# Kernel tuning notes

Measured on AMD Instinct MI355X. Metric: run time of the kernel, lower is better.

## Reference

```python
import jax, jax.numpy as jnp
import numpy as np

N, D, E, R = 50000, 128, 640000, 500
BN_EPS = 1e-3  # keras BatchNormalization default
L2_EPS = 1e-12  # tf.nn.l2_normalize default


def setup_inputs() -> dict:
    key = jax.random.key(0)
    ks = jax.random.split(key, 10)
    rows = jnp.sort(jax.random.randint(ks[0], (E,), 0, N, dtype=jnp.int32))
    cols = jax.random.randint(ks[1], (E,), 0, N, dtype=jnp.int32)
    return {
        "x": jax.random.normal(ks[2], (N, D), dtype=jnp.float32),
        "rows": rows,
        "cols": cols,
        "adj_vals": jax.random.uniform(ks[3], (E,), dtype=jnp.float32),
        "rel_ids": jax.random.randint(ks[4], (E,), 0, R, dtype=jnp.int32),
        "gamma1": jnp.ones((D,), jnp.float32),
        "beta1": jnp.zeros((D,), jnp.float32),
        "mean1": jnp.zeros((D,), jnp.float32),
        "var1": jnp.ones((D,), jnp.float32),
        "W1": jax.random.normal(ks[5], (D, D), dtype=jnp.float32) * 0.05,
        "b1": jnp.zeros((D,), jnp.float32),
        "gamma2": jnp.ones((D,), jnp.float32),
        "beta2": jnp.zeros((D,), jnp.float32),
        "mean2": jnp.zeros((D,), jnp.float32),
        "var2": jnp.ones((D,), jnp.float32),
        "relation_coeffs": jax.random.uniform(ks[6], (R,), dtype=jnp.float32),
        "coeff_kernel": jax.random.normal(ks[7], (N, 1), dtype=jnp.float32) * 0.05,
        "Wd": jax.random.normal(ks[8], (D, D), dtype=jnp.float32) * 0.05,
        "bd": jnp.zeros((D,), jnp.float32),
    }


def _bn(h, gamma, beta, mean, var):
    # keras BatchNormalization, inference mode (moving stats)
    return (h - mean) * jax.lax.rsqrt(var + BN_EPS) * gamma + beta


def _spmm(vals, rows, cols, h, n):
    # sparse [n,n] @ dense [n,d]: gather source rows, weight, scatter-add to dest
    return jax.ops.segment_sum(vals[:, None] * h[cols], rows, num_segments=n)


def _l2n(a):
    # tf.nn.l2_normalize(a, axis=1)
    sq = jnp.sum(a * a, axis=1, keepdims=True)
    return a * jax.lax.rsqrt(jnp.maximum(sq, L2_EPS))


def reference(x, rows, cols, adj_vals, rel_ids,
              gamma1, beta1, mean1, var1, W1, b1,
              gamma2, beta2, mean2, var2,
              relation_coeffs, coeff_kernel, Wd, bd):
    n = x.shape[0]
    # ---- agg1: alinet_gcn: tanh(A @ (BN(x) @ W1) + b1) ----
    h = _bn(x, gamma1, beta1, mean1, var1)
    y1 = jnp.tanh(_spmm(adj_vals, rows, cols, h @ W1, n) + b1)
    # ---- agg2: Rgin ----
    h2 = _bn(y1, gamma2, beta2, mean2, var2)
    # relation-weighted edge values: A.values / (rel_coeffs[values] + 1)
    ev = adj_vals / (relation_coeffs[rel_ids] + 1.0)
    agg = _spmm(ev, rows, cols, h2, n)
    self_term = h2 * (coeff_kernel + 1.0)  # CoeffLayer(mul=True)
    y2 = (agg + self_term) @ Wd + bd       # Dense(dim)
    # ---- output: concat of per-layer l2-normalized embeddings, renormalized ----
    y = jnp.concatenate([_l2n(x), _l2n(y1), _l2n(y2)], axis=1)
    return _l2n(y)
```

## Files before the change

kernel.cpp:

```cpp
#include <hip/hip_runtime.h>
#include <math.h>

#define D 128
#define BN_EPS 1e-3f
#define L2_EPS 1e-12f
#define AGG_S 136
#define OUT_S 392

typedef unsigned int uint;
typedef unsigned short ushort;
typedef __attribute__((ext_vector_type(8))) short bf16x8;
typedef __attribute__((ext_vector_type(4))) float f32x4;

__device__ __forceinline__ ushort f2bf(float f) {
  uint u = __float_as_uint(f);
  uint r = (u + 0x7fffu + ((u >> 16) & 1u)) >> 16;
  return (ushort)r;
}
__device__ __forceinline__ float bflo(uint u) { return __uint_as_float(u << 16); }
__device__ __forceinline__ float bfhi(uint u) { return __uint_as_float(u & 0xffff0000u); }
__device__ __forceinline__ float bf2f(ushort h) { return __uint_as_float(((uint)h) << 16); }

__device__ __forceinline__ void pack_bfrag_block(
    const float* __restrict__ W, const float* __restrict__ gamma,
    const float* __restrict__ var, ushort* __restrict__ Bf, int blk, int tid) {
  int t = blk * 256 + tid;
  int f = t >> 6, lane = t & 63;
  int kc = f >> 3, nt = f & 7, q = lane >> 4, m = lane & 15;
  ushort tmp[8];
#pragma unroll
  for (int j = 0; j < 8; ++j) {
    int k = kc * 32 + q * 8 + j;
    float s = gamma[k] * rsqrtf(var[k] + BN_EPS);
    tmp[j] = f2bf(s * W[k * D + nt * 16 + m]);
  }
  uint4 o;
  o.x = (uint)tmp[0] | ((uint)tmp[1] << 16);
  o.y = (uint)tmp[2] | ((uint)tmp[3] << 16);
  o.z = (uint)tmp[4] | ((uint)tmp[5] << 16);
  o.w = (uint)tmp[6] | ((uint)tmp[7] << 16);
  reinterpret_cast<uint4*>(Bf)[t] = o;
}

__device__ __forceinline__ void bn_bias_block(
    const float* __restrict__ W, const float* __restrict__ gamma,
    const float* __restrict__ beta, const float* __restrict__ mean,
    const float* __restrict__ var, float* __restrict__ outb, int j) {
  float acc = 0.f;
  for (int k = 0; k < D; ++k) {
    float s = gamma[k] * rsqrtf(var[k] + BN_EPS);
    float sh = beta[k] - mean[k] * s;
    acc += sh * W[k * D + j];
  }
  outb[j] = acc;
}

__global__ __launch_bounds__(256) void prep_kernel(
    const float* __restrict__ x, ushort* __restrict__ xbf, int n4,
    const int* __restrict__ rows, int* __restrict__ row_ptr, int n, int e,
    const float* __restrict__ W1, const float* __restrict__ g1,
    const float* __restrict__ v1, ushort* __restrict__ Bf1,
    const float* __restrict__ Wd, const float* __restrict__ g2,
    const float* __restrict__ v2, ushort* __restrict__ Bf2,
    const float* __restrict__ beta1, const float* __restrict__ mean1,
    float* __restrict__ bnb,
    const float* __restrict__ beta2, const float* __restrict__ mean2,
    float* __restrict__ shd,
    const int* __restrict__ cols, const float* __restrict__ adj,
    const int* __restrict__ rel, const float* __restrict__ relc,
    uint2* __restrict__ ew1, uint2* __restrict__ ew2,
    int nbConv, int nbRp) {
  const int b = blockIdx.x, tid = threadIdx.x;
  if (b < nbConv) {
    int i = b * 256 + tid;
    if (i < n4) {
      float4 v = reinterpret_cast<const float4*>(x)[i];
      ushort4 o;
      o.x = f2bf(v.x); o.y = f2bf(v.y); o.z = f2bf(v.z); o.w = f2bf(v.w);
      reinterpret_cast<ushort4*>(xbf)[i] = o;
    }
    return;
  }
  int bb = b - nbConv;
  if (bb < nbRp) {
    int i = bb * 256 + tid;
    if (i <= n) {
      int lo = 0, hi = e;
      while (lo < hi) {
        int mid = (lo + hi) >> 1;
        if (rows[mid] < i) lo = mid + 1; else hi = mid;
      }
      row_ptr[i] = lo;
    }
    return;
  }
  bb -= nbRp;
  if (bb < 8) { pack_bfrag_block(W1, g1, v1, Bf1, bb, tid); return; }
  if (bb < 16) { pack_bfrag_block(Wd, g2, v2, Bf2, bb - 8, tid); return; }
  if (bb == 16) { if (tid < D) bn_bias_block(W1, g1, beta1, mean1, v1, bnb, tid); return; }
  if (bb == 17) { if (tid < D) bn_bias_block(Wd, g2, beta2, mean2, v2, shd, tid); return; }
  int i = (bb - 18) * 256 + tid;
  if (i < e) {
    uint c = (uint)cols[i];
    float a = adj[i];
    ew1[i] = make_uint2(c, __float_as_uint(a));
    float w2 = a / (relc[rel[i]] + 1.0f);
    ew2[i] = make_uint2(c, __float_as_uint(w2));
  } else if (i == e) {
    ew1[i] = make_uint2(0u, 0u);
    ew2[i] = make_uint2(0u, 0u);
  }
}

template <bool SELF>
__device__ __forceinline__ float spmm_rows(
    const uint4* __restrict__ S4, const int* __restrict__ row_ptr,
    const uint2* __restrict__ ew, const float* __restrict__ ck,
    int r, int n, int lane, float acc[8]) {
  const int m = lane & 15;
  const int g16 = lane & 48;
  const int rr = r < n ? r : n - 1;
  const int e0 = row_ptr[rr];
  int len = row_ptr[rr + 1] - e0;
  if (r >= n) len = 0;
  int mx = len;
  mx = max(mx, __shfl_xor(mx, 16));
  mx = max(mx, __shfl_xor(mx, 32));
  const int lastOff = len > 0 ? len - 1 : 0;

#pragma unroll
  for (int j = 0; j < 8; ++j) acc[j] = 0.f;
  float ws = 0.f;

  for (int base = 0; base < mx; base += 16) {
    const int mo = base + m;
    const uint2 mym = ew[e0 + (mo < len ? mo : lastOff)];
    const float myw = (mo < len) ? __uint_as_float(mym.y) : 0.f;
#pragma unroll
    for (int h = 0; h < 2; ++h) {
      if (base + h * 8 >= mx) break;
      uint4 gv[8];
      float wv[8];
#pragma unroll
      for (int u = 0; u < 8; ++u) {
        const int src = g16 + h * 8 + u;
        const uint cidx = (uint)__shfl((int)mym.x, src);
        wv[u] = __shfl(myw, src);
        gv[u] = S4[(size_t)cidx * 16 + m];
      }
#pragma unroll
      for (int u = 0; u < 8; ++u) {
        const float w = wv[u];
        ws += w;
        acc[0] = fmaf(w, bflo(gv[u].x), acc[0]);
        acc[1] = fmaf(w, bfhi(gv[u].x), acc[1]);
        acc[2] = fmaf(w, bflo(gv[u].y), acc[2]);
        acc[3] = fmaf(w, bfhi(gv[u].y), acc[3]);
        acc[4] = fmaf(w, bflo(gv[u].z), acc[4]);
        acc[5] = fmaf(w, bfhi(gv[u].z), acc[5]);
        acc[6] = fmaf(w, bflo(gv[u].w), acc[6]);
        acc[7] = fmaf(w, bfhi(gv[u].w), acc[7]);
      }
    }
  }

  if (SELF && r < n) {
    uint4 us = S4[(size_t)rr * 16 + m];
    float cp = ck[rr] + 1.0f;
    acc[0] = fmaf(cp, bflo(us.x), acc[0]);
    acc[1] = fmaf(cp, bfhi(us.x), acc[1]);
    acc[2] = fmaf(cp, bflo(us.y), acc[2]);
    acc[3] = fmaf(cp, bfhi(us.y), acc[3]);
    acc[4] = fmaf(cp, bflo(us.z), acc[4]);
    acc[5] = fmaf(cp, bfhi(us.z), acc[5]);
    acc[6] = fmaf(cp, bflo(us.w), acc[6]);
    acc[7] = fmaf(cp, bfhi(us.w), acc[7]);
  }
  return ws;
}

__device__ __forceinline__ uint4 pack_acc(const float acc[8]) {
  uint4 o;
  o.x = (uint)f2bf(acc[0]) | ((uint)f2bf(acc[1]) << 16);
  o.y = (uint)f2bf(acc[2]) | ((uint)f2bf(acc[3]) << 16);
  o.z = (uint)f2bf(acc[4]) | ((uint)f2bf(acc[5]) << 16);
  o.w = (uint)f2bf(acc[6]) | ((uint)f2bf(acc[7]) << 16);
  return o;
}

__global__ __launch_bounds__(256) void spmm_gemm1_kernel(
    const ushort* __restrict__ src, const int* __restrict__ row_ptr,
    const uint2* __restrict__ ew, const ushort* __restrict__ Bf,
    const float* __restrict__ bnb, const float* __restrict__ b1,
    ushort* __restrict__ y1, int n) {
  __shared__ ushort aggT[16 * AGG_S];
  __shared__ ushort y1T[16 * AGG_S];
  __shared__ float rsL[16];

  const int tid = threadIdx.x;
  const int wave = tid >> 6, lane = tid & 63;
  const int g = lane >> 4, m = lane & 15;
  const int rloc = wave * 4 + g;
  const int r = blockIdx.x * 16 + rloc;

  float acc[8];
  float ws = spmm_rows<false>(reinterpret_cast<const uint4*>(src), row_ptr,
                              ew, nullptr, r, n, lane, acc);
  *reinterpret_cast<uint4*>(&aggT[rloc * AGG_S + m * 8]) = pack_acc(acc);
  if (m == 0) rsL[rloc] = ws;
  __syncthreads();

  const bf16x8* Bv = reinterpret_cast<const bf16x8*>(Bf);
  bf16x8 af[4];
#pragma unroll
  for (int kc = 0; kc < 4; ++kc)
    af[kc] = *reinterpret_cast<const bf16x8*>(&aggT[m * AGG_S + kc * 32 + g * 8]);

  f32x4 acc2[2];
  acc2[0] = (f32x4){0.f, 0.f, 0.f, 0.f};
  acc2[1] = (f32x4){0.f, 0.f, 0.f, 0.f};
  const int nt0 = wave * 2;
#pragma unroll
  for (int kc = 0; kc < 4; ++kc) {
#pragma unroll
    for (int t = 0; t < 2; ++t) {
      bf16x8 b = Bv[(kc * 8 + nt0 + t) * 64 + lane];
      acc2[t] = __builtin_amdgcn_mfma_f32_16x16x32_bf16(b, af[kc], acc2[t], 0, 0, 0);
    }
  }

  const float rs = rsL[m];
#pragma unroll
  for (int t = 0; t < 2; ++t) {
    const int c = (nt0 + t) * 16 + g * 4;
    const float4 bn = *reinterpret_cast<const float4*>(&bnb[c]);
    const float4 bb = *reinterpret_cast<const float4*>(&b1[c]);
    ushort4 ov;
    ov.x = f2bf(tanhf(acc2[t][0] + rs * bn.x + bb.x));
    ov.y = f2bf(tanhf(acc2[t][1] + rs * bn.y + bb.y));
    ov.z = f2bf(tanhf(acc2[t][2] + rs * bn.z + bb.z));
    ov.w = f2bf(tanhf(acc2[t][3] + rs * bn.w + bb.w));
    *reinterpret_cast<ushort4*>(&y1T[m * AGG_S + c]) = ov;
  }
  __syncthreads();

  const int row = tid >> 4, col = tid & 15;
  uint4 v = *reinterpret_cast<const uint4*>(&y1T[row * AGG_S + col * 8]);
  const size_t gi = (size_t)blockIdx.x * 256 + tid;
  if ((int)(gi >> 4) < n) reinterpret_cast<uint4*>(y1)[gi] = v;
}

__global__ __launch_bounds__(256) void spmm_gemm2_kernel(
    const ushort* __restrict__ src , const int* __restrict__ row_ptr,
    const uint2* __restrict__ ew, const ushort* __restrict__ Bf,
    const float* __restrict__ shd, const float* __restrict__ bd,
    const float* __restrict__ ck, const float* __restrict__ x,
    float* __restrict__ out, int n) {
  __shared__ __align__(16) char smemRaw[16 * OUT_S * 4];
  __shared__ float rsL[16];
  __shared__ float sp0[4][16], sp1[4][16], sp2[4][16];
  ushort* aggT = reinterpret_cast<ushort*>(smemRaw);
  float* outT = reinterpret_cast<float*>(smemRaw);

  const int tid = threadIdx.x;
  const int wave = tid >> 6, lane = tid & 63;
  const int g = lane >> 4, m = lane & 15;
  const int rloc = wave * 4 + g;
  const int r = blockIdx.x * 16 + rloc;

  float acc[8];
  float ws = spmm_rows<true>(reinterpret_cast<const uint4*>(src), row_ptr,
                             ew, ck, r, n, lane, acc);
  *reinterpret_cast<uint4*>(&aggT[rloc * AGG_S + m * 8]) = pack_acc(acc);
  if (m == 0) rsL[rloc] = ws;
  __syncthreads();

  const bf16x8* Bv = reinterpret_cast<const bf16x8*>(Bf);
  bf16x8 af[4];
#pragma unroll
  for (int kc = 0; kc < 4; ++kc)
    af[kc] = *reinterpret_cast<const bf16x8*>(&aggT[m * AGG_S + kc * 32 + g * 8]);

  f32x4 acc2[2];
  acc2[0] = (f32x4){0.f, 0.f, 0.f, 0.f};
  acc2[1] = (f32x4){0.f, 0.f, 0.f, 0.f};
  const int nt0 = wave * 2;
#pragma unroll
  for (int kc = 0; kc < 4; ++kc) {
#pragma unroll
    for (int t = 0; t < 2; ++t) {
      bf16x8 b = Bv[(kc * 8 + nt0 + t) * 64 + lane];
      acc2[t] = __builtin_amdgcn_mfma_f32_16x16x32_bf16(b, af[kc], acc2[t], 0, 0, 0);
    }
  }

  const int rm = min(blockIdx.x * 16 + m, n - 1);
  const int c0 = wave * 32 + g * 8;
  const float4 xv0 = *reinterpret_cast<const float4*>(&x[(size_t)rm * D + c0]);
  const float4 xv1 = *reinterpret_cast<const float4*>(&x[(size_t)rm * D + c0 + 4]);
  const uint4 yv = *reinterpret_cast<const uint4*>(&src[(size_t)rm * D + c0]);
  const float ya = bflo(yv.x), yb = bfhi(yv.x), yc = bflo(yv.y), yd = bfhi(yv.y);
  const float ye = bflo(yv.z), yf = bfhi(yv.z), yg = bflo(yv.w), yh = bfhi(yv.w);

  float s0p = xv0.x * xv0.x + xv0.y * xv0.y + xv0.z * xv0.z + xv0.w * xv0.w +
              xv1.x * xv1.x + xv1.y * xv1.y + xv1.z * xv1.z + xv1.w * xv1.w;
  float s1p = ya * ya + yb * yb + yc * yc + yd * yd +
              ye * ye + yf * yf + yg * yg + yh * yh;

  const float rbias = rsL[m] + ck[rm] + 1.0f;
  float s2p = 0.f;
#pragma unroll
  for (int t = 0; t < 2; ++t) {
    const int c = (nt0 + t) * 16 + g * 4;
    const float4 sh = *reinterpret_cast<const float4*>(&shd[c]);
    const float4 bb = *reinterpret_cast<const float4*>(&bd[c]);
    acc2[t][0] += rbias * sh.x + bb.x;
    acc2[t][1] += rbias * sh.y + bb.y;
    acc2[t][2] += rbias * sh.z + bb.z;
    acc2[t][3] += rbias * sh.w + bb.w;
    s2p += acc2[t][0] * acc2[t][0] + acc2[t][1] * acc2[t][1] +
           acc2[t][2] * acc2[t][2] + acc2[t][3] * acc2[t][3];
  }

  s0p += __shfl_xor(s0p, 16); s0p += __shfl_xor(s0p, 32);
  s1p += __shfl_xor(s1p, 16); s1p += __shfl_xor(s1p, 32);
  s2p += __shfl_xor(s2p, 16); s2p += __shfl_xor(s2p, 32);
  if (lane < 16) { sp0[wave][lane] = s0p; sp1[wave][lane] = s1p; sp2[wave][lane] = s2p; }
  __syncthreads();

  const float s0 = sp0[0][m] + sp0[1][m] + sp0[2][m] + sp0[3][m];
  const float s1 = sp1[0][m] + sp1[1][m] + sp1[2][m] + sp1[3][m];
  const float s2 = sp2[0][m] + sp2[1][m] + sp2[2][m] + sp2[3][m];
  const float i0 = 1.0f / sqrtf(fmaxf(s0, L2_EPS));
  const float i1 = 1.0f / sqrtf(fmaxf(s1, L2_EPS));
  const float i2 = 1.0f / sqrtf(fmaxf(s2, L2_EPS));
  const float tot = s0 * i0 * i0 + s1 * i1 * i1 + s2 * i2 * i2;
  const float sc = 1.0f / sqrtf(fmaxf(tot, L2_EPS));
  const float f0 = i0 * sc, f1 = i1 * sc, f2 = i2 * sc;

  float* orow = &outT[m * OUT_S];
  *reinterpret_cast<float4*>(&orow[c0]) =
      make_float4(xv0.x * f0, xv0.y * f0, xv0.z * f0, xv0.w * f0);
  *reinterpret_cast<float4*>(&orow[c0 + 4]) =
      make_float4(xv1.x * f0, xv1.y * f0, xv1.z * f0, xv1.w * f0);
  *reinterpret_cast<float4*>(&orow[128 + c0]) =
      make_float4(ya * f1, yb * f1, yc * f1, yd * f1);
  *reinterpret_cast<float4*>(&orow[128 + c0 + 4]) =
      make_float4(ye * f1, yf * f1, yg * f1, yh * f1);
#pragma unroll
  for (int t = 0; t < 2; ++t) {
    const int c = (nt0 + t) * 16 + g * 4;
    *reinterpret_cast<float4*>(&orow[256 + c]) =
        make_float4(acc2[t][0] * f2, acc2[t][1] * f2, acc2[t][2] * f2, acc2[t][3] * f2);
  }
  __syncthreads();

#pragma unroll
  for (int it = 0; it < 6; ++it) {
    const int idx = it * 256 + tid;
    const int rw = idx / 96, cc = idx % 96;
    float4 v = *reinterpret_cast<const float4*>(&outT[rw * OUT_S + cc * 4]);
    const int gr = blockIdx.x * 16 + rw;
    if (gr < n) reinterpret_cast<float4*>(out)[(size_t)gr * 96 + cc] = v;
  }
}

extern "C" void kernel_launch(void* const* d_in, const int* in_sizes, int n_in,
                              void* d_out, int out_size, void* d_ws, size_t ws_size,
                              hipStream_t stream) {
  const float* x      = (const float*)d_in[0];
  const int*   rows   = (const int*)d_in[1];
  const int*   cols   = (const int*)d_in[2];
  const float* adj    = (const float*)d_in[3];
  const int*   rel    = (const int*)d_in[4];
  const float* gamma1 = (const float*)d_in[5];
  const float* beta1  = (const float*)d_in[6];
  const float* mean1  = (const float*)d_in[7];
  const float* var1   = (const float*)d_in[8];
  const float* W1     = (const float*)d_in[9];
  const float* b1     = (const float*)d_in[10];
  const float* gamma2 = (const float*)d_in[11];
  const float* beta2  = (const float*)d_in[12];
  const float* mean2  = (const float*)d_in[13];
  const float* var2   = (const float*)d_in[14];
  const float* relc   = (const float*)d_in[15];
  const float* ck     = (const float*)d_in[16];
  const float* Wd     = (const float*)d_in[17];
  const float* bd     = (const float*)d_in[18];
  float* out = (float*)d_out;

  const int n = in_sizes[0] / D;
  const int e = in_sizes[1];
  size_t nd = (size_t)n * D;

  char* p = (char*)d_ws;
  ushort* xbf   = (ushort*)p; p += nd * 2;
  ushort* y1bf  = (ushort*)p; p += nd * 2;
  ushort* Bf1   = (ushort*)p; p += 32768;
  ushort* Bf2   = (ushort*)p; p += 32768;
  float*  bnb   = (float*)p;  p += 512;
  float*  shd   = (float*)p;  p += 512;
  p = (char*)(((uintptr_t)p + 15) & ~(uintptr_t)15);
  uint2* ew1    = (uint2*)p;  p += (size_t)(e + 1) * 8;
  uint2* ew2    = (uint2*)p;  p += (size_t)(e + 1) * 8;
  int* row_ptr  = (int*)p;    p += (size_t)(n + 1) * 4;

  const int n4 = (int)(nd / 4);
  const int nbConv = (n4 + 255) / 256;
  const int nbRp = (n + 1 + 255) / 256;
  const int nbEw = (e + 1 + 255) / 256;
  const int nbPrep = nbConv + nbRp + 18 + nbEw;

  prep_kernel<<<nbPrep, 256, 0, stream>>>(
      x, xbf, n4, rows, row_ptr, n, e,
      W1, gamma1, var1, Bf1, Wd, gamma2, var2, Bf2,
      beta1, mean1, bnb, beta2, mean2, shd,
      cols, adj, rel, relc, ew1, ew2, nbConv, nbRp);

  const int fblocks = (n + 15) / 16;
  spmm_gemm1_kernel<<<fblocks, 256, 0, stream>>>(
      xbf, row_ptr, ew1, Bf1, bnb, b1, y1bf, n);
  spmm_gemm2_kernel<<<fblocks, 256, 0, stream>>>(
      y1bf, row_ptr, ew2, Bf2, shd, bd, ck, x, out, n);
}
```

Measured before the change: 213.8 us.

## Sort rows by degree so each wave handles rows of similar length

```diff
diff --git a/kernel.cpp b/kernel.cpp
--- a/kernel.cpp
+++ b/kernel.cpp
@@ -57,7 +57,8 @@
 
 __global__ __launch_bounds__(256) void prep_kernel(
     const float* __restrict__ x, ushort* __restrict__ xbf, int n4,
-    const int* __restrict__ rows, int* __restrict__ row_ptr, int n, int e,
+    const int* __restrict__ rows, int* __restrict__ row_ptr,
+    uint* __restrict__ hist, int n, int e,
     const float* __restrict__ W1, const float* __restrict__ g1,
     const float* __restrict__ v1, ushort* __restrict__ Bf1,
     const float* __restrict__ Wd, const float* __restrict__ g2,
@@ -91,6 +92,14 @@
         if (rows[mid] < i) lo = mid + 1; else hi = mid;
       }
       row_ptr[i] = lo;
+      if (i < n) {
+        int lo2 = lo, hi2 = e;
+        while (lo2 < hi2) {
+          int mid = (lo2 + hi2) >> 1;
+          if (rows[mid] < i + 1) lo2 = mid + 1; else hi2 = mid;
+        }
+        atomicAdd(&hist[min(lo2 - lo, 255)], 1u);
+      }
     }
     return;
   }
@@ -112,17 +121,54 @@
   }
 }
 
+__global__ __launch_bounds__(256) void scan_kernel(
+    const uint* __restrict__ hist, uint* __restrict__ binoff) {
+  __shared__ uint s[256];
+  const int t = threadIdx.x;
+  const uint c = hist[t];
+  s[t] = c;
+  __syncthreads();
+  for (int off = 1; off < 256; off <<= 1) {
+    uint v = (t + off < 256) ? s[t + off] : 0u;
+    __syncthreads();
+    s[t] += v;
+    __syncthreads();
+  }
+  binoff[t] = s[t] - c;
+}
+
+__global__ __launch_bounds__(256) void scatter_kernel(
+    const int* __restrict__ row_ptr, uint* __restrict__ binoff,
+    int* __restrict__ perm, int n) {
+  __shared__ uint lcnt[256], lbase[256], lrk[256];
+  const int t = threadIdx.x;
+  lcnt[t] = 0u; lrk[t] = 0u;
+  __syncthreads();
+  const int i = (int)blockIdx.x * 256 + t;
+  int dg = -1;
+  if (i < n) {
+    dg = min(row_ptr[i + 1] - row_ptr[i], 255);
+    atomicAdd(&lcnt[dg], 1u);
+  }
+  __syncthreads();
+  if (lcnt[t] > 0u) lbase[t] = atomicAdd(&binoff[t], lcnt[t]);
+  __syncthreads();
+  if (i < n) {
+    uint rk = atomicAdd(&lrk[dg], 1u);
+    perm[lbase[dg] + rk] = i;
+  }
+}
+
 template <bool SELF>
 __device__ __forceinline__ float spmm_rows(
     const uint4* __restrict__ S4, const int* __restrict__ row_ptr,
     const uint2* __restrict__ ew, const float* __restrict__ ck,
-    int r, int n, int lane, float acc[8]) {
+    int r, bool valid, int lane, float acc[8]) {
   const int m = lane & 15;
   const int g16 = lane & 48;
-  const int rr = r < n ? r : n - 1;
-  const int e0 = row_ptr[rr];
-  int len = row_ptr[rr + 1] - e0;
-  if (r >= n) len = 0;
+  const int e0 = row_ptr[r];
+  int len = row_ptr[r + 1] - e0;
+  if (!valid) len = 0;
   int mx = len;
   mx = max(mx, __shfl_xor(mx, 16));
   mx = max(mx, __shfl_xor(mx, 32));
@@ -164,9 +210,9 @@
     }
   }
 
-  if (SELF && r < n) {
-    uint4 us = S4[(size_t)rr * 16 + m];
-    float cp = ck[rr] + 1.0f;
+  if (SELF && valid) {
+    uint4 us = S4[(size_t)r * 16 + m];
+    float cp = ck[r] + 1.0f;
     acc[0] = fmaf(cp, bflo(us.x), acc[0]);
     acc[1] = fmaf(cp, bfhi(us.x), acc[1]);
     acc[2] = fmaf(cp, bflo(us.y), acc[2]);
@@ -192,20 +238,27 @@
     const ushort* __restrict__ src, const int* __restrict__ row_ptr,
     const uint2* __restrict__ ew, const ushort* __restrict__ Bf,
     const float* __restrict__ bnb, const float* __restrict__ b1,
-    ushort* __restrict__ y1, int n) {
+    const int* __restrict__ perm, ushort* __restrict__ y1, int n) {
   __shared__ ushort aggT[16 * AGG_S];
   __shared__ ushort y1T[16 * AGG_S];
   __shared__ float rsL[16];
+  __shared__ int permL[16];
 
   const int tid = threadIdx.x;
   const int wave = tid >> 6, lane = tid & 63;
   const int g = lane >> 4, m = lane & 15;
   const int rloc = wave * 4 + g;
-  const int r = blockIdx.x * 16 + rloc;
+  const int idx = (int)blockIdx.x * 16 + rloc;
+  const bool valid = idx < n;
+  if (tid < 16) {
+    int pi = (int)blockIdx.x * 16 + tid;
+    permL[tid] = perm[pi < n ? pi : n - 1];
+  }
+  const int r = perm[valid ? idx : n - 1];
 
   float acc[8];
   float ws = spmm_rows<false>(reinterpret_cast<const uint4*>(src), row_ptr,
-                              ew, nullptr, r, n, lane, acc);
+                              ew, nullptr, r, valid, lane, acc);
   *reinterpret_cast<uint4*>(&aggT[rloc * AGG_S + m * 8]) = pack_acc(acc);
   if (m == 0) rsL[rloc] = ws;
   __syncthreads();
@@ -246,8 +299,9 @@
 
   const int row = tid >> 4, col = tid & 15;
   uint4 v = *reinterpret_cast<const uint4*>(&y1T[row * AGG_S + col * 8]);
-  const size_t gi = (size_t)blockIdx.x * 256 + tid;
-  if ((int)(gi >> 4) < n) reinterpret_cast<uint4*>(y1)[gi] = v;
+  const int gidx = (int)blockIdx.x * 16 + row;
+  if (gidx < n)
+    reinterpret_cast<uint4*>(y1)[(size_t)permL[row] * 16 + col] = v;
 }
 
 __global__ __launch_bounds__(256) void spmm_gemm2_kernel(
@@ -255,10 +309,11 @@
     const uint2* __restrict__ ew, const ushort* __restrict__ Bf,
     const float* __restrict__ shd, const float* __restrict__ bd,
     const float* __restrict__ ck, const float* __restrict__ x,
-    float* __restrict__ out, int n) {
+    const int* __restrict__ perm, float* __restrict__ out, int n) {
   __shared__ __align__(16) char smemRaw[16 * OUT_S * 4];
   __shared__ float rsL[16];
   __shared__ float sp0[4][16], sp1[4][16], sp2[4][16];
+  __shared__ int permL[16];
   ushort* aggT = reinterpret_cast<ushort*>(smemRaw);
   float* outT = reinterpret_cast<float*>(smemRaw);
 
@@ -266,11 +321,17 @@
   const int wave = tid >> 6, lane = tid & 63;
   const int g = lane >> 4, m = lane & 15;
   const int rloc = wave * 4 + g;
-  const int r = blockIdx.x * 16 + rloc;
+  const int idx = (int)blockIdx.x * 16 + rloc;
+  const bool valid = idx < n;
+  if (tid < 16) {
+    int pi = (int)blockIdx.x * 16 + tid;
+    permL[tid] = perm[pi < n ? pi : n - 1];
+  }
+  const int r = perm[valid ? idx : n - 1];
 
   float acc[8];
   float ws = spmm_rows<true>(reinterpret_cast<const uint4*>(src), row_ptr,
-                             ew, ck, r, n, lane, acc);
+                             ew, ck, r, valid, lane, acc);
   *reinterpret_cast<uint4*>(&aggT[rloc * AGG_S + m * 8]) = pack_acc(acc);
   if (m == 0) rsL[rloc] = ws;
   __syncthreads();
@@ -294,7 +355,7 @@
     }
   }
 
-  const int rm = min(blockIdx.x * 16 + m, n - 1);
+  const int rm = permL[m];
   const int c0 = wave * 32 + g * 8;
   const float4 xv0 = *reinterpret_cast<const float4*>(&x[(size_t)rm * D + c0]);
   const float4 xv1 = *reinterpret_cast<const float4*>(&x[(size_t)rm * D + c0 + 4]);
@@ -357,11 +418,12 @@
 
 #pragma unroll
   for (int it = 0; it < 6; ++it) {
-    const int idx = it * 256 + tid;
-    const int rw = idx / 96, cc = idx % 96;
+    const int ii = it * 256 + tid;
+    const int rw = ii / 96, cc = ii % 96;
     float4 v = *reinterpret_cast<const float4*>(&outT[rw * OUT_S + cc * 4]);
-    const int gr = blockIdx.x * 16 + rw;
-    if (gr < n) reinterpret_cast<float4*>(out)[(size_t)gr * 96 + cc] = v;
+    const int gidx = (int)blockIdx.x * 16 + rw;
+    if (gidx < n)
+      reinterpret_cast<float4*>(out)[(size_t)permL[rw] * 96 + cc] = v;
   }
 }
 
@@ -404,6 +466,9 @@
   uint2* ew1    = (uint2*)p;  p += (size_t)(e + 1) * 8;
   uint2* ew2    = (uint2*)p;  p += (size_t)(e + 1) * 8;
   int* row_ptr  = (int*)p;    p += (size_t)(n + 1) * 4;
+  uint* hist    = (uint*)p;   p += 1024;
+  uint* binoff  = (uint*)p;   p += 1024;
+  int* perm     = (int*)p;    p += (size_t)n * 4;
 
   const int n4 = (int)(nd / 4);
   const int nbConv = (n4 + 255) / 256;
@@ -411,15 +476,20 @@
   const int nbEw = (e + 1 + 255) / 256;
   const int nbPrep = nbConv + nbRp + 18 + nbEw;
 
+  (void)hipMemsetAsync(hist, 0, 256 * sizeof(uint), stream);
+
   prep_kernel<<<nbPrep, 256, 0, stream>>>(
-      x, xbf, n4, rows, row_ptr, n, e,
+      x, xbf, n4, rows, row_ptr, hist, n, e,
       W1, gamma1, var1, Bf1, Wd, gamma2, var2, Bf2,
       beta1, mean1, bnb, beta2, mean2, shd,
       cols, adj, rel, relc, ew1, ew2, nbConv, nbRp);
 
+  scan_kernel<<<1, 256, 0, stream>>>(hist, binoff);
+  scatter_kernel<<<(n + 255) / 256, 256, 0, stream>>>(row_ptr, binoff, perm, n);
+
   const int fblocks = (n + 15) / 16;
   spmm_gemm1_kernel<<<fblocks, 256, 0, stream>>>(
-      xbf, row_ptr, ew1, Bf1, bnb, b1, y1bf, n);
+      xbf, row_ptr, ew1, Bf1, bnb, b1, perm, y1bf, n);
   spmm_gemm2_kernel<<<fblocks, 256, 0, stream>>>(
-      y1bf, row_ptr, ew2, Bf2, shd, bd, ck, x, out, n);
-}
+      y1bf, row_ptr, ew2, Bf2, shd, bd, ck, x, perm, out, n);
+}
```

Measured after the change: 361.3 us. 1.69x slower.
